# Optimization experiments

Hardware: AMD Instinct MI355X
Metric: run time of the kernel (lower is better)

The kernel has to match this reference:

```python
import jax, jax.numpy as jnp
import numpy as np

N_IN, C, T, E, N_OUT, F = 50000, 64, 8, 800000, 50000, 64


def setup_inputs() -> dict:
    key = jax.random.key(0)
    k0, k1, k2, k3, k4 = jax.random.split(key, 5)
    node_features = jax.random.normal(k0, (N_IN, C), dtype=jnp.float32)
    edge_features = jax.random.normal(k1, (T, E), dtype=jnp.float32)
    idx_out = jax.random.randint(k2, (E,), 0, N_OUT)
    idx_in = jax.random.randint(k3, (E,), 0, N_IN)
    indices = jnp.stack([idx_out, idx_in], axis=1).astype(jnp.int64)  # [E, 2]
    # glorot-ish scale for kernel [T, C, F]
    scale = np.sqrt(2.0 / (C + F)).astype(np.float32)
    kernel = jax.random.normal(k4, (T, C, F), dtype=jnp.float32) * scale
    bias = jnp.zeros((F,), dtype=jnp.float32)
    return {
        "node_features": node_features,
        "edge_features": edge_features,
        "indices": indices,
        "kernel": kernel,
        "bias": bias,
        "out_size": N_OUT,
    }


def reference(node_features, edge_features, indices, kernel, bias, out_size):
    # sparse_conv (combine='unstack'):
    #   out[i] = sum_t ( segment_sum_{e: out(e)=i} ef[t,e] * x[in(e)] ) @ kernel[t] + bias
    gathered = node_features[indices[:, 1]]          # [E, C] irregular gather
    seg_ids = indices[:, 0]
    n_terms = kernel.shape[0]                        # small fixed structural dim
    out = jnp.zeros((out_size, kernel.shape[2]), dtype=node_features.dtype)
    for t in range(n_terms):
        weighted = edge_features[t][:, None] * gathered            # [E, C]
        agg = jax.ops.segment_sum(weighted, seg_ids, num_segments=out_size)  # [No, C]
        out = out + agg @ kernel[t]                                # [No, F]
    return out + bias
```

## Files before the change

### kernel.cpp

```cpp
#include <hip/hip_runtime.h>

constexpr int N_IN  = 50000;
constexpr int C     = 64;
constexpr int T     = 8;
constexpr int E     = 800000;
constexpr int N_OUT = 50000;
constexpr int F     = 64;

constexpr int CHUNK   = 4096;
constexpr int NCHUNK  = (E + CHUNK - 1) / CHUNK;
constexpr int NBIN_S  = (N_OUT + 255) / 256;
constexpr int LEN_CNT = NBIN_S * NCHUNK;
constexpr int SCA     = (LEN_CNT + 255) / 256;

constexpr size_t OFF_NFBF  = 0;
constexpr size_t OFF_KT    = 6400000;
constexpr size_t OFF_CNT   = OFF_KT + 65536;
constexpr size_t OFF_BSUM  = OFF_CNT + 153664;
constexpr size_t OFF_START = OFF_BSUM + 1024;
constexpr size_t OFF_EFH   = OFF_START + 200064;
constexpr size_t OFF_ENT   = OFF_EFH + 12800000;
constexpr size_t OFF_ENT2  = OFF_ENT + 6400000;
static_assert(OFF_EFH % 16 == 0 && OFF_ENT % 16 == 0 && OFF_ENT2 % 16 == 0,
              "alignment");

typedef __attribute__((ext_vector_type(8))) short short8;
typedef __attribute__((ext_vector_type(4))) float f32x4;
typedef __attribute__((ext_vector_type(8))) _Float16 f16x8;

__device__ inline unsigned short f2bf(float x) {
    unsigned int u = __float_as_uint(x);
    unsigned int r = (u + 0x7FFFu + ((u >> 16) & 1u)) >> 16;
    return (unsigned short)r;
}
__device__ inline float bf2f(unsigned short u) {
    return __uint_as_float(((unsigned int)u) << 16);
}

constexpr int NF_BLOCKS = N_IN * C / 4 / 256;
constexpr int KT_BLOCKS = 32;
constexpr int ET_BLOCKS = E / 256;
constexpr int BH_BLOCKS = NCHUNK;

__global__ __launch_bounds__(256) void prep_kernel(const float* __restrict__ nf,
                                                   const float* __restrict__ Kmat,
                                                   const float* __restrict__ ef,
                                                   const int* __restrict__ idx,
                                                   unsigned short* __restrict__ nf_bf,
                                                   unsigned short* __restrict__ K_T,
                                                   _Float16* __restrict__ efh,
                                                   int* __restrict__ counts) {
    __shared__ int hist[NBIN_S];
    const int b   = blockIdx.x;
    const int tid = threadIdx.x;

    if (b < NF_BLOCKS) {
        int i = b * 256 + tid;
        float4 v = ((const float4*)nf)[i];
        unsigned int u0 = (unsigned int)f2bf(v.x) | ((unsigned int)f2bf(v.y) << 16);
        unsigned int u1 = (unsigned int)f2bf(v.z) | ((unsigned int)f2bf(v.w) << 16);
        ((uint2*)nf_bf)[i] = make_uint2(u0, u1);
    } else if (b < NF_BLOCKS + KT_BLOCKS) {
        for (int k = (b - NF_BLOCKS) * 256 + tid; k < T * C * F; k += KT_BLOCKS * 256) {
            int f = k & 63;
            int c = (k >> 6) & 63;
            int t = k >> 12;
            K_T[f * 512 + t * 64 + c] = f2bf(Kmat[k]);
        }
    } else if (b < NF_BLOCKS + KT_BLOCKS + ET_BLOCKS) {
        int e = (b - NF_BLOCKS - KT_BLOCKS) * 256 + tid;
        f16x8 h;
#pragma unroll
        for (int t = 0; t < T; ++t)
            h[t] = (_Float16)ef[(size_t)t * E + e];
        *(f16x8*)(efh + (size_t)e * 8) = h;
    } else {
        const int c = b - NF_BLOCKS - KT_BLOCKS - ET_BLOCKS;
        for (int i = tid; i < NBIN_S; i += 256) hist[i] = 0;
        __syncthreads();
        const int e0 = c * CHUNK;
        const int n  = min(CHUNK, E - e0);
        for (int i = tid; i < n; i += 256) {
            int o = ((const int2*)idx)[e0 + i].x;
            atomicAdd(&hist[o >> 8], 1);
        }
        __syncthreads();
        for (int i = tid; i < NBIN_S; i += 256)
            counts[i * NCHUNK + c] = hist[i];
    }
}

__global__ __launch_bounds__(256) void scanA_kernel(int* __restrict__ a,
                                                    int* __restrict__ bsum) {
    __shared__ int sh[256];
    const int tid = threadIdx.x;
    int g = blockIdx.x * 256 + tid;
    int v = (g < LEN_CNT) ? a[g] : 0;
    sh[tid] = v;
    __syncthreads();
#pragma unroll
    for (int off = 1; off < 256; off <<= 1) {
        int x = 0;
        if (tid >= off) x = sh[tid - off];
        __syncthreads();
        if (tid >= off) sh[tid] += x;
        __syncthreads();
    }
    int incl = sh[tid];
    if (g < LEN_CNT) a[g] = incl - v;
    if (tid == 255) bsum[blockIdx.x] = incl;
}

__global__ __launch_bounds__(256) void scanBC_kernel(int* __restrict__ a,
                                                     const int* __restrict__ bsum) {
    __shared__ int sh[256];
    const int bi  = blockIdx.x;
    const int tid = threadIdx.x;
    sh[tid] = (tid < bi) ? bsum[tid] : 0;
    __syncthreads();
#pragma unroll
    for (int off = 128; off >= 1; off >>= 1) {
        if (tid < off) sh[tid] += sh[tid + off];
        __syncthreads();
    }
    const int offset = sh[0];
    int g = bi * 256 + tid;
    if (g < LEN_CNT) a[g] += offset;
}

__global__ __launch_bounds__(512) void binscatter_kernel(const int* __restrict__ idx,
                                                         const int* __restrict__ offs,
                                                         uint2* __restrict__ ent) {
    __shared__ int cur[NBIN_S];
    const int tid = threadIdx.x;
    const int c   = blockIdx.x;
    for (int i = tid; i < NBIN_S; i += 512) cur[i] = offs[i * NCHUNK + c];
    __syncthreads();
    const int e0 = c * CHUNK;
    const int n  = min(CHUNK, E - e0);
    for (int i = tid; i < n; i += 512) {
        int2 oi = ((const int2*)idx)[e0 + i];
        int bin = oi.x >> 8;
        int loc = oi.x & 255;
        int pos = atomicAdd(&cur[bin], 1);
        ent[pos] = make_uint2(((unsigned)loc << 20) | (unsigned)(e0 + i),
                              (unsigned)oi.y);
    }
}

__global__ __launch_bounds__(512) void permfix_kernel(const int* __restrict__ offs,
                                                      const uint2* __restrict__ ent,
                                                      int* __restrict__ start_g,
                                                      uint2* __restrict__ ent2) {
    __shared__ int hist[256];
    __shared__ int sc[256];
    __shared__ int cur[256];
    const int tid = threadIdx.x;
    const int b   = blockIdx.x;
    const int W0  = offs[b * NCHUNK];
    const int W1  = (b + 1 < NBIN_S) ? offs[(b + 1) * NCHUNK] : E;

    if (tid < 256) hist[tid] = 0;
    __syncthreads();
    for (int i = W0 + tid; i < W1; i += 512)
        atomicAdd(&hist[ent[i].x >> 20], 1);
    __syncthreads();

    if (tid < 256) sc[tid] = hist[tid];
    __syncthreads();
    for (int off = 1; off < 256; off <<= 1) {
        int x = 0;
        if (tid < 256 && tid >= off) x = sc[tid - off];
        __syncthreads();
        if (tid < 256 && tid >= off) sc[tid] += x;
        __syncthreads();
    }
    if (tid < 256) {
        int s = W0 + sc[tid] - hist[tid];
        int g = b * 256 + tid;
        if (g < N_OUT) start_g[g] = s;
        cur[tid] = s;
    }
    if (b == NBIN_S - 1 && tid == 0) start_g[N_OUT] = E;
    __syncthreads();

    for (int i = W0 + tid; i < W1; i += 512) {
        uint2 u = ent[i];
        int loc = (int)(u.x >> 20);
        int e   = (int)(u.x & 0xFFFFFu);
        int pos = atomicAdd(&cur[loc], 1);
        ent2[pos] = make_uint2(u.y, (unsigned)e);
    }
}

__global__ __launch_bounds__(256) void aggregate_kernel(const unsigned short* __restrict__ nf_bf,
                                                        const unsigned short* __restrict__ K_T,
                                                        const int* __restrict__ start,
                                                        const uint2* __restrict__ ent2,
                                                        const _Float16* __restrict__ efh,
                                                        const float* __restrict__ bias,
                                                        float* __restrict__ out) {
    __shared__ unsigned short A_lds[16][520];

    const int wave = threadIdx.x >> 6;
    const int lane = threadIdx.x & 63;
    const int node_base = blockIdx.x * 16;

    const unsigned long long* ent2q = (const unsigned long long*)ent2;
    const f16x8* efh8 = (const f16x8*)efh;

    for (int q = 0; q < 4; ++q) {
        const int m = wave * 4 + q;
        const int o = node_base + m;
        const int s0 = __builtin_amdgcn_readfirstlane(start[o]);
        const int s1 = __builtin_amdgcn_readfirstlane(start[o + 1]);

        float acc[8] = {0.f, 0.f, 0.f, 0.f, 0.f, 0.f, 0.f, 0.f};

        for (int base = s0; base < s1; base += 64) {
            const int cnt = min(64, s1 - base);
            unsigned long long v = 0;
            if (base + lane < s1)
                v = __builtin_nontemporal_load(ent2q + base + lane);
            int iv = (int)(unsigned)(v & 0xFFFFFFFFull);
            int ev = (int)(unsigned)(v >> 32);

            int j = 0;
            for (; j + 4 <= cnt; j += 4) {
                const int i0 = __builtin_amdgcn_readlane(iv, j + 0);
                const int i1 = __builtin_amdgcn_readlane(iv, j + 1);
                const int i2 = __builtin_amdgcn_readlane(iv, j + 2);
                const int i3 = __builtin_amdgcn_readlane(iv, j + 3);
                float x0 = bf2f(nf_bf[(size_t)i0 * 64 + lane]);
                float x1 = bf2f(nf_bf[(size_t)i1 * 64 + lane]);
                float x2 = bf2f(nf_bf[(size_t)i2 * 64 + lane]);
                float x3 = bf2f(nf_bf[(size_t)i3 * 64 + lane]);
                f16x8 w0 = efh8[(size_t)__builtin_amdgcn_readlane(ev, j + 0)];
                f16x8 w1 = efh8[(size_t)__builtin_amdgcn_readlane(ev, j + 1)];
                f16x8 w2 = efh8[(size_t)__builtin_amdgcn_readlane(ev, j + 2)];
                f16x8 w3 = efh8[(size_t)__builtin_amdgcn_readlane(ev, j + 3)];
#pragma unroll
                for (int t = 0; t < T; ++t) {
                    acc[t] += (float)w0[t] * x0;
                    acc[t] += (float)w1[t] * x1;
                    acc[t] += (float)w2[t] * x2;
                    acc[t] += (float)w3[t] * x3;
                }
            }
            for (; j < cnt; ++j) {
                const int i0 = __builtin_amdgcn_readlane(iv, j);
                float x0 = bf2f(nf_bf[(size_t)i0 * 64 + lane]);
                f16x8 w0 = efh8[(size_t)__builtin_amdgcn_readlane(ev, j)];
#pragma unroll
                for (int t = 0; t < T; ++t) acc[t] += (float)w0[t] * x0;
            }
        }

#pragma unroll
        for (int t = 0; t < T; ++t) A_lds[m][t * 64 + lane] = f2bf(acc[t]);
    }
    __syncthreads();

    const int mrow = lane & 15;
    const int kb   = lane >> 4;
    const int fcol = wave * 16 + mrow;

    f32x4 acc4 = {0.f, 0.f, 0.f, 0.f};
#pragma unroll
    for (int s = 0; s < 16; ++s) {
        const int k0 = s * 32 + kb * 8;
        short8 a = *(const short8*)&A_lds[mrow][k0];
        short8 b = *(const short8*)(K_T + (size_t)fcol * 512 + k0);
        acc4 = __builtin_amdgcn_mfma_f32_16x16x32_bf16(a, b, acc4, 0, 0, 0);
    }

    const float bv = bias[fcol];
#pragma unroll
    for (int r = 0; r < 4; ++r) {
        const int m = kb * 4 + r;
        __builtin_nontemporal_store(acc4[r] + bv,
                                    &out[(size_t)(node_base + m) * F + fcol]);
    }
}

extern "C" void kernel_launch(void* const* d_in, const int* in_sizes, int n_in,
                              void* d_out, int out_size, void* d_ws, size_t ws_size,
                              hipStream_t stream) {
    const float* nf   = (const float*)d_in[0];
    const float* ef   = (const float*)d_in[1];
    const int*   idx  = (const int*)d_in[2];
    const float* Kmat = (const float*)d_in[3];
    const float* bias = (const float*)d_in[4];
    float*       out  = (float*)d_out;

    char* ws = (char*)d_ws;
    unsigned short* nf_bf  = (unsigned short*)(ws + OFF_NFBF);
    unsigned short* K_T    = (unsigned short*)(ws + OFF_KT);
    int*            counts = (int*)(ws + OFF_CNT);
    int*            bsum   = (int*)(ws + OFF_BSUM);
    int*            start  = (int*)(ws + OFF_START);
    _Float16*       efh    = (_Float16*)(ws + OFF_EFH);
    uint2*          ent    = (uint2*)(ws + OFF_ENT);
    uint2*          ent2   = (uint2*)(ws + OFF_ENT2);

    prep_kernel<<<NF_BLOCKS + KT_BLOCKS + ET_BLOCKS + BH_BLOCKS, 256, 0, stream>>>(
        nf, Kmat, ef, idx, nf_bf, K_T, efh, counts);
    scanA_kernel<<<SCA, 256, 0, stream>>>(counts, bsum);
    scanBC_kernel<<<SCA, 256, 0, stream>>>(counts, bsum);
    binscatter_kernel<<<NCHUNK, 512, 0, stream>>>(idx, counts, ent);
    permfix_kernel<<<NBIN_S, 512, 0, stream>>>(counts, ent, start, ent2);
    aggregate_kernel<<<N_OUT / 16, 256, 0, stream>>>(
        nf_bf, K_T, start, ent2, efh, bias, out);
}
```

Measured before the change: 181.7 us.

## Pack edge entries to 32 bits and pre-bin edge weights for locality

Binscatter now also copies each edge's f16x8 weight vector into a bin-ordered buffer. Entries shrink to 32-bit words (16-bit in-node index plus 16-bit within-bin offset), which halves index traffic in permfix and aggregate. The aggregate kernel reads weights from the bin-local buffer instead of scattered global edge positions, remaps block IDs in an XCD-aware pattern, and uses plain stores for the output. The cost is an extra 12.8MB weight write in binscatter, and the 16-bit packing relies on N_IN fitting in 16 bits and on bins holding at most 65536 entries.

```diff
diff --git a/kernel.cpp b/kernel.cpp
--- a/kernel.cpp
+++ b/kernel.cpp
@@ -20,9 +20,9 @@
 constexpr size_t OFF_START = OFF_BSUM + 1024;
 constexpr size_t OFF_EFH   = OFF_START + 200064;
 constexpr size_t OFF_ENT   = OFF_EFH + 12800000;
-constexpr size_t OFF_ENT2  = OFF_ENT + 6400000;
-static_assert(OFF_EFH % 16 == 0 && OFF_ENT % 16 == 0 && OFF_ENT2 % 16 == 0,
-              "alignment");
+constexpr size_t OFF_ENT2  = OFF_ENT + 3200000;
+constexpr size_t OFF_BINW  = OFF_ENT2 + 3200000;
+static_assert(OFF_EFH % 16 == 0 && OFF_BINW % 16 == 0, "alignment");
 
 typedef __attribute__((ext_vector_type(8))) short short8;
 typedef __attribute__((ext_vector_type(4))) float f32x4;
@@ -130,10 +130,14 @@
 
 __global__ __launch_bounds__(512) void binscatter_kernel(const int* __restrict__ idx,
                                                          const int* __restrict__ offs,
-                                                         uint2* __restrict__ ent) {
+                                                         const _Float16* __restrict__ efh,
+                                                         unsigned* __restrict__ ent,
+                                                         _Float16* __restrict__ binw) {
     __shared__ int cur[NBIN_S];
     const int tid = threadIdx.x;
     const int c   = blockIdx.x;
+    const f16x8* efh8 = (const f16x8*)efh;
+    f16x8* binw8 = (f16x8*)binw;
     for (int i = tid; i < NBIN_S; i += 512) cur[i] = offs[i * NCHUNK + c];
     __syncthreads();
     const int e0 = c * CHUNK;
@@ -142,16 +146,17 @@
         int2 oi = ((const int2*)idx)[e0 + i];
         int bin = oi.x >> 8;
         int loc = oi.x & 255;
+        f16x8 w = efh8[e0 + i];
         int pos = atomicAdd(&cur[bin], 1);
-        ent[pos] = make_uint2(((unsigned)loc << 20) | (unsigned)(e0 + i),
-                              (unsigned)oi.y);
+        ent[pos]   = ((unsigned)loc << 16) | (unsigned)oi.y;
+        binw8[pos] = w;
     }
 }
 
 __global__ __launch_bounds__(512) void permfix_kernel(const int* __restrict__ offs,
-                                                      const uint2* __restrict__ ent,
+                                                      const unsigned* __restrict__ ent,
                                                       int* __restrict__ start_g,
-                                                      uint2* __restrict__ ent2) {
+                                                      unsigned* __restrict__ ent2) {
     __shared__ int hist[256];
     __shared__ int sc[256];
     __shared__ int cur[256];
@@ -163,7 +168,7 @@
     if (tid < 256) hist[tid] = 0;
     __syncthreads();
     for (int i = W0 + tid; i < W1; i += 512)
-        atomicAdd(&hist[ent[i].x >> 20], 1);
+        atomicAdd(&hist[ent[i] >> 16], 1);
     __syncthreads();
 
     if (tid < 256) sc[tid] = hist[tid];
@@ -185,29 +190,35 @@
     __syncthreads();
 
     for (int i = W0 + tid; i < W1; i += 512) {
-        uint2 u = ent[i];
-        int loc = (int)(u.x >> 20);
-        int e   = (int)(u.x & 0xFFFFFu);
+        unsigned u = ent[i];
+        int loc = (int)(u >> 16);
         int pos = atomicAdd(&cur[loc], 1);
-        ent2[pos] = make_uint2(u.y, (unsigned)e);
+        ent2[pos] = ((unsigned)(i - W0) << 16) | (u & 0xFFFFu);
     }
 }
 
 __global__ __launch_bounds__(256) void aggregate_kernel(const unsigned short* __restrict__ nf_bf,
                                                         const unsigned short* __restrict__ K_T,
                                                         const int* __restrict__ start,
-                                                        const uint2* __restrict__ ent2,
-                                                        const _Float16* __restrict__ efh,
+                                                        const unsigned* __restrict__ ent2,
+                                                        const _Float16* __restrict__ binw,
+                                                        const int* __restrict__ offs,
                                                         const float* __restrict__ bias,
                                                         float* __restrict__ out) {
     __shared__ unsigned short A_lds[16][520];
 
+    constexpr int NWG = N_OUT / 16;
+    constexpr int Q = NWG / 8, R = NWG % 8;
+    const int xc = blockIdx.x & 7;
+    const int sl = blockIdx.x >> 3;
+    const int orig = (xc < R ? xc * (Q + 1) : R * (Q + 1) + (xc - R) * Q) + sl;
+
     const int wave = threadIdx.x >> 6;
     const int lane = threadIdx.x & 63;
-    const int node_base = blockIdx.x * 16;
-
-    const unsigned long long* ent2q = (const unsigned long long*)ent2;
-    const f16x8* efh8 = (const f16x8*)efh;
+    const int node_base = orig * 16;
+    const int Wbase = offs[(orig >> 4) * NCHUNK];
+
+    const f16x8* binw8 = (const f16x8*)binw;
 
     for (int q = 0; q < 4; ++q) {
         const int m = wave * 4 + q;
@@ -219,26 +230,22 @@
 
         for (int base = s0; base < s1; base += 64) {
             const int cnt = min(64, s1 - base);
-            unsigned long long v = 0;
-            if (base + lane < s1)
-                v = __builtin_nontemporal_load(ent2q + base + lane);
-            int iv = (int)(unsigned)(v & 0xFFFFFFFFull);
-            int ev = (int)(unsigned)(v >> 32);
+            int vv = (base + lane < s1) ? (int)ent2[base + lane] : 0;
 
             int j = 0;
             for (; j + 4 <= cnt; j += 4) {
-                const int i0 = __builtin_amdgcn_readlane(iv, j + 0);
-                const int i1 = __builtin_amdgcn_readlane(iv, j + 1);
-                const int i2 = __builtin_amdgcn_readlane(iv, j + 2);
-                const int i3 = __builtin_amdgcn_readlane(iv, j + 3);
-                float x0 = bf2f(nf_bf[(size_t)i0 * 64 + lane]);
-                float x1 = bf2f(nf_bf[(size_t)i1 * 64 + lane]);
-                float x2 = bf2f(nf_bf[(size_t)i2 * 64 + lane]);
-                float x3 = bf2f(nf_bf[(size_t)i3 * 64 + lane]);
-                f16x8 w0 = efh8[(size_t)__builtin_amdgcn_readlane(ev, j + 0)];
-                f16x8 w1 = efh8[(size_t)__builtin_amdgcn_readlane(ev, j + 1)];
-                f16x8 w2 = efh8[(size_t)__builtin_amdgcn_readlane(ev, j + 2)];
-                f16x8 w3 = efh8[(size_t)__builtin_amdgcn_readlane(ev, j + 3)];
+                const int v0 = __builtin_amdgcn_readlane(vv, j + 0);
+                const int v1 = __builtin_amdgcn_readlane(vv, j + 1);
+                const int v2 = __builtin_amdgcn_readlane(vv, j + 2);
+                const int v3 = __builtin_amdgcn_readlane(vv, j + 3);
+                float x0 = bf2f(nf_bf[(size_t)(v0 & 0xFFFF) * 64 + lane]);
+                float x1 = bf2f(nf_bf[(size_t)(v1 & 0xFFFF) * 64 + lane]);
+                float x2 = bf2f(nf_bf[(size_t)(v2 & 0xFFFF) * 64 + lane]);
+                float x3 = bf2f(nf_bf[(size_t)(v3 & 0xFFFF) * 64 + lane]);
+                f16x8 w0 = binw8[(size_t)(Wbase + (v0 >> 16))];
+                f16x8 w1 = binw8[(size_t)(Wbase + (v1 >> 16))];
+                f16x8 w2 = binw8[(size_t)(Wbase + (v2 >> 16))];
+                f16x8 w3 = binw8[(size_t)(Wbase + (v3 >> 16))];
 #pragma unroll
                 for (int t = 0; t < T; ++t) {
                     acc[t] += (float)w0[t] * x0;
@@ -248,9 +255,9 @@
                 }
             }
             for (; j < cnt; ++j) {
-                const int i0 = __builtin_amdgcn_readlane(iv, j);
-                float x0 = bf2f(nf_bf[(size_t)i0 * 64 + lane]);
-                f16x8 w0 = efh8[(size_t)__builtin_amdgcn_readlane(ev, j)];
+                const int v0 = __builtin_amdgcn_readlane(vv, j);
+                float x0 = bf2f(nf_bf[(size_t)(v0 & 0xFFFF) * 64 + lane]);
+                f16x8 w0 = binw8[(size_t)(Wbase + (v0 >> 16))];
 #pragma unroll
                 for (int t = 0; t < T; ++t) acc[t] += (float)w0[t] * x0;
             }
@@ -278,8 +285,7 @@
 #pragma unroll
     for (int r = 0; r < 4; ++r) {
         const int m = kb * 4 + r;
-        __builtin_nontemporal_store(acc4[r] + bv,
-                                    &out[(size_t)(node_base + m) * F + fcol]);
+        out[(size_t)(node_base + m) * F + fcol] = acc4[r] + bv;
     }
 }
 
@@ -300,15 +306,16 @@
     int*            bsum   = (int*)(ws + OFF_BSUM);
     int*            start  = (int*)(ws + OFF_START);
     _Float16*       efh    = (_Float16*)(ws + OFF_EFH);
-    uint2*          ent    = (uint2*)(ws + OFF_ENT);
-    uint2*          ent2   = (uint2*)(ws + OFF_ENT2);
+    unsigned*       ent    = (unsigned*)(ws + OFF_ENT);
+    unsigned*       ent2   = (unsigned*)(ws + OFF_ENT2);
+    _Float16*       binw   = (_Float16*)(ws + OFF_BINW);
 
     prep_kernel<<<NF_BLOCKS + KT_BLOCKS + ET_BLOCKS + BH_BLOCKS, 256, 0, stream>>>(
         nf, Kmat, ef, idx, nf_bf, K_T, efh, counts);
     scanA_kernel<<<SCA, 256, 0, stream>>>(counts, bsum);
     scanBC_kernel<<<SCA, 256, 0, stream>>>(counts, bsum);
-    binscatter_kernel<<<NCHUNK, 512, 0, stream>>>(idx, counts, ent);
+    binscatter_kernel<<<NCHUNK, 512, 0, stream>>>(idx, counts, efh, ent, binw);
     permfix_kernel<<<NBIN_S, 512, 0, stream>>>(counts, ent, start, ent2);
     aggregate_kernel<<<N_OUT / 16, 256, 0, stream>>>(
-        nf_bf, K_T, start, ent2, efh, bias, out);
-}
+        nf_bf, K_T, start, ent2, binw, counts, bias, out);
+}
```

Result: no change. 184.1 us (+1.3%).
